# Kernel tuning notes

Measured on AMD Instinct MI355X. Metric: run time of the kernel, lower is better.

## Reference

```python
import jax, jax.numpy as jnp
import numpy as np

N = 100000   # nodes
E = 800000   # directed edges (before self-loops)
D = 256      # in_feats == out_feats


def setup_inputs() -> dict:
    key = jax.random.key(0)
    ks = jax.random.split(key, 6)
    scale = 1.0 / np.sqrt(D)
    features = jax.random.normal(ks[0], (N, D), dtype=jnp.float32)
    src = jax.random.randint(ks[1], (E,), 0, N, dtype=jnp.int32)
    dst = jax.random.randint(ks[2], (E,), 0, N, dtype=jnp.int32)
    W1 = jax.random.normal(ks[3], (D, D), dtype=jnp.float32) * scale
    b1 = jnp.zeros((D,), dtype=jnp.float32)
    W2 = jax.random.normal(ks[4], (D, D), dtype=jnp.float32) * scale
    b2 = jnp.zeros((D,), dtype=jnp.float32)
    return {"features": features, "src": src, "dst": dst,
            "W1": W1, "b1": b1, "W2": W2, "b2": b2}


def _graph_conv(h, src, dst, norm_src, norm_dst, W, b):
    # DGL GraphConv, norm='both': out = D_in^{-1/2} A (D_out^{-1/2} h W) + b
    h = (h * norm_src) @ W            # [N, D] project (W first; in==out)
    agg = jax.ops.segment_sum(h[src], dst, num_segments=N)  # SpMM gather-scatter
    return agg * norm_dst + b


def reference(features, src, dst, W1, b1, W2, b2):
    # forward does g = dgl.add_self_loop(g)
    loops = jnp.arange(N, dtype=src.dtype)
    s = jnp.concatenate([src, loops])
    d = jnp.concatenate([dst, loops])
    ones = jnp.ones_like(s, dtype=jnp.float32)
    deg_out = jax.ops.segment_sum(ones, s, num_segments=N)   # out-degree (src side)
    deg_in = jax.ops.segment_sum(ones, d, num_segments=N)    # in-degree  (dst side)
    norm_src = jnp.where(deg_out > 0, deg_out ** -0.5, 0.0)[:, None]
    norm_dst = jnp.where(deg_in > 0, deg_in ** -0.5, 0.0)[:, None]
    x = _graph_conv(features, s, d, norm_src, norm_dst, W1, b1)
    x = jax.nn.relu(x)
    x = _graph_conv(x, s, d, norm_src, norm_dst, W2, b2)
    return x
```

## Files before the change

### kernel.cpp

```cpp
#include <hip/hip_runtime.h>

#define NN 100000
#define DD 256
#define SCAN_BLK 1024

typedef unsigned int uint;
typedef unsigned short ushort;
typedef __attribute__((ext_vector_type(8))) short bfx8;
typedef __attribute__((ext_vector_type(4))) float fx4;

__device__ __forceinline__ ushort f2bf(float f) {
    uint u = __float_as_uint(f);
    u += 0x7fff + ((u >> 16) & 1);
    return (ushort)(u >> 16);
}

__device__ __forceinline__ uint cvtpk(float lo, float hi) {
    uint r;
    asm("v_cvt_pk_bf16_f32 %0, %1, %2" : "=v"(r) : "v"(lo), "v"(hi));
    return r;
}

__global__ __launch_bounds__(256) void k_count(const int* __restrict__ src,
                                               const int* __restrict__ dst, int E,
                                               int* __restrict__ dego,
                                               int* __restrict__ degi) {
    int e = blockIdx.x * 256 + threadIdx.x;
    if (e < E) {
        atomicAdd(&dego[src[e]], 1);
        atomicAdd(&degi[dst[e]], 1);
    }
}

__global__ __launch_bounds__(256) void k_norm(const int* __restrict__ dego,
                                              const int* __restrict__ degi,
                                              float* __restrict__ ns,
                                              float* __restrict__ nd) {
    int i = blockIdx.x * 256 + threadIdx.x;
    if (i < NN) {
        ns[i] = rsqrtf((float)(dego[i] + 1));
        nd[i] = rsqrtf((float)(degi[i] + 1));
    }
}

__device__ __forceinline__ int block_scan_inc(int v, int* sm) {
    int t = threadIdx.x;
    sm[t] = v;
    __syncthreads();
    for (int o = 1; o < SCAN_BLK; o <<= 1) {
        int x = (t >= o) ? sm[t - o] : 0;
        __syncthreads();
        sm[t] += x;
        __syncthreads();
    }
    return sm[t];
}

__global__ __launch_bounds__(SCAN_BLK) void k_scan1(const int* __restrict__ degi,
                                                    int* __restrict__ partials) {
    __shared__ int sm[SCAN_BLK];
    int i = blockIdx.x * SCAN_BLK + threadIdx.x;
    int v = (i < NN) ? degi[i] : 0;
    block_scan_inc(v, sm);
    if (threadIdx.x == 0) partials[blockIdx.x] = sm[SCAN_BLK - 1];
}

__global__ __launch_bounds__(128) void k_scan2(int* __restrict__ partials, int nb) {
    __shared__ int sm[128];
    int t = threadIdx.x;
    int v = (t < nb) ? partials[t] : 0;
    sm[t] = v;
    __syncthreads();
    for (int o = 1; o < 128; o <<= 1) {
        int x = (t >= o) ? sm[t - o] : 0;
        __syncthreads();
        sm[t] += x;
        __syncthreads();
    }
    if (t < nb) partials[t] = sm[t] - v;
}

__global__ __launch_bounds__(SCAN_BLK) void k_scan3(const int* __restrict__ degi,
                                                    const int* __restrict__ partials,
                                                    int* __restrict__ rowptr,
                                                    int* __restrict__ cursor) {
    __shared__ int sm[SCAN_BLK];
    int i = blockIdx.x * SCAN_BLK + threadIdx.x;
    int v = (i < NN) ? degi[i] : 0;
    int incl = block_scan_inc(v, sm);
    int excl = partials[blockIdx.x] + incl - v;
    if (i <= NN) rowptr[i] = excl;
    if (i < NN) cursor[i] = excl;
}

__global__ __launch_bounds__(256) void k_fill(const int* __restrict__ src,
                                              const int* __restrict__ dst, int E,
                                              int* __restrict__ cursor,
                                              int* __restrict__ eidx) {
    int e = blockIdx.x * 256 + threadIdx.x;
    if (e < E) {
        int d = dst[e];
        int p = atomicAdd(&cursor[d], 1);
        eidx[p] = src[e];
    }
}

__global__ __launch_bounds__(256) void k_convW(const float* __restrict__ W1,
                                               const float* __restrict__ W2,
                                               ushort* __restrict__ Wt1,
                                               ushort* __restrict__ Wt2) {
    int n = blockIdx.x & 255, k = threadIdx.x;
    const float* W = (blockIdx.x < 256) ? W1 : W2;
    ushort* Wt = (blockIdx.x < 256) ? Wt1 : Wt2;
    Wt[n * DD + k] = f2bf(W[(size_t)k * DD + n]);
}

template <bool FP32A>
__global__ __launch_bounds__(512, 4) void k_mfgemm(const void* __restrict__ Av,
                                                   const float* __restrict__ nrm,
                                                   const ushort* __restrict__ Wt,
                                                   ushort* __restrict__ H) {
    constexpr int CPR = FP32A ? 16 : 8;
    constexpr int CALLS = (128 * CPR) / (8 * 64);
    __shared__ uint4 atq[2][128 * CPR];
    int t = threadIdx.x;
    int brow = blockIdx.x * 128;
    int lane = t & 63, w = t >> 6;
    int wr = w >> 2, wc = w & 3;
    int lg = lane >> 4, lr = lane & 15;

    uint gofs[CALLS];
#pragma unroll
    for (int i = 0; i < CALLS; ++i) {
        int slot = (w * CALLS + i) * 64;
        int r = slot / CPR + lane / CPR;
        int cs = (lane % CPR) ^ (r & 7);
        int row = brow + r;
        if (row >= NN) row = NN - 1;
        if (FP32A)
            gofs[i] = (uint)(((size_t)row * DD + cs * 4) * 4);
        else
            gofs[i] = (uint)(((size_t)row * DD + cs * 8) * 2);
    }

    auto stage = [&](int buf, int ks) {
#pragma unroll
        for (int i = 0; i < CALLS; ++i) {
            int slot = (w * CALLS + i) * 64;
            const char* g = (const char*)Av + gofs[i] + ks * (FP32A ? 256 : 128);
            __builtin_amdgcn_global_load_lds(
                (const __attribute__((address_space(1))) uint*)g,
                (__attribute__((address_space(3))) uint*)&atq[buf][slot], 16, 0, 0);
        }
    };

    const uint4* wb[4];
#pragma unroll
    for (int ni = 0; ni < 4; ++ni)
        wb[ni] = (const uint4*)(Wt + (size_t)(wc * 64 + ni * 16 + lr) * DD);

    bfx8 bfr2[2][4];
    auto ldB = [&](int ks) {
#pragma unroll
        for (int kk = 0; kk < 2; ++kk)
#pragma unroll
            for (int ni = 0; ni < 4; ++ni)
                bfr2[kk][ni] = *(const bfx8*)&wb[ni][ks * 8 + kk * 4 + lg];
    };

    fx4 acc[4][4];
#pragma unroll
    for (int mi = 0; mi < 4; ++mi)
#pragma unroll
        for (int ni = 0; ni < 4; ++ni)
            acc[mi][ni] = (fx4){0.f, 0.f, 0.f, 0.f};

    stage(0, 0);
    ldB(0);
    __syncthreads();

    int buf = 0;
#pragma unroll
    for (int ks = 0; ks < 4; ++ks) {
        if (ks < 3) stage(buf ^ 1, ks + 1);
#pragma unroll
        for (int kk = 0; kk < 2; ++kk) {
#pragma unroll
            for (int mi = 0; mi < 4; ++mi) {
                int r = wr * 64 + mi * 16 + lr;
                bfx8 af;
                if (FP32A) {
                    int cf = (kk * 4 + lg) * 2;
                    fx4 q0 = *(const fx4*)&atq[buf][r * 16 + (cf ^ (r & 7))];
                    fx4 q1 = *(const fx4*)&atq[buf][r * 16 + ((cf + 1) ^ (r & 7))];
                    uint4 uu;
                    uu.x = cvtpk(q0.x, q0.y);
                    uu.y = cvtpk(q0.z, q0.w);
                    uu.z = cvtpk(q1.x, q1.y);
                    uu.w = cvtpk(q1.z, q1.w);
                    af = *(bfx8*)&uu;
                } else {
                    int c = kk * 4 + lg;
                    af = *(const bfx8*)&atq[buf][r * 8 + (c ^ (r & 7))];
                }
#pragma unroll
                for (int ni = 0; ni < 4; ++ni)
                    acc[mi][ni] = __builtin_amdgcn_mfma_f32_16x16x32_bf16(
                        af, bfr2[kk][ni], acc[mi][ni], 0, 0, 0);
            }
        }
        if (ks < 3) ldB(ks + 1);
        __syncthreads();
        buf ^= 1;
    }

    float scl[4][4];
    if (FP32A) {
#pragma unroll
        for (int mi = 0; mi < 4; ++mi)
#pragma unroll
            for (int j = 0; j < 4; ++j) {
                int row = brow + wr * 64 + mi * 16 + lg * 4 + j;
                scl[mi][j] = nrm[row < NN ? row : NN - 1];
            }
    }
    ushort* hs = (ushort*)&atq[0][0];
#pragma unroll
    for (int h = 0; h < 2; ++h) {
        if (wr == h) {
#pragma unroll
            for (int mi = 0; mi < 4; ++mi)
#pragma unroll
                for (int ni = 0; ni < 4; ++ni)
#pragma unroll
                    for (int j = 0; j < 4; ++j) {
                        int rl = mi * 16 + lg * 4 + j;
                        int c = wc * 64 + ni * 16 + lr;
                        float v = acc[mi][ni][j];
                        if (FP32A) v *= scl[mi][j];
                        hs[rl * 256 + (((c >> 3) ^ (rl & 7)) << 3) + (c & 7)] =
                            f2bf(v);
                    }
        }
        __syncthreads();
        {
            int rl = t >> 3;
            int grow = brow + h * 64 + rl;
            if (grow < NN) {
                ushort* hp = H + (size_t)grow * DD;
#pragma unroll
                for (int i = 0; i < 4; ++i) {
                    int ch = (t & 7) + i * 8;
                    uint4 v = *(const uint4*)&hs[rl * 256 + ((ch ^ (rl & 7)) << 3)];
                    *(uint4*)(hp + ch * 8) = v;
                }
            }
        }
        __syncthreads();
    }
}

__global__ __launch_bounds__(256) void k_spmm_bf(const ushort* __restrict__ T,
                                                 const int* __restrict__ rowptr,
                                                 const int* __restrict__ eidx,
                                                 const float* __restrict__ nd,
                                                 const float* __restrict__ ns,
                                                 const float* __restrict__ bias,
                                                 ushort* __restrict__ obf,
                                                 float* __restrict__ of,
                                                 int layer1) {
    int wid = threadIdx.x >> 6, lane = threadIdx.x & 63;
    int node = blockIdx.x * 4 + wid;
    if (node >= NN) return;
    int c = lane << 2;
    uint2 sv = *(const uint2*)(T + (size_t)node * DD + c);
    float p0[4], p1[4], p2[4], p3[4];
    p0[0] = __uint_as_float(sv.x << 16);
    p0[1] = __uint_as_float(sv.x & 0xffff0000u);
    p0[2] = __uint_as_float(sv.y << 16);
    p0[3] = __uint_as_float(sv.y & 0xffff0000u);
#pragma unroll
    for (int j = 0; j < 4; ++j) { p1[j] = 0.f; p2[j] = 0.f; p3[j] = 0.f; }
    int e = rowptr[node], end = rowptr[node + 1];
    for (; e + 3 < end; e += 4) {
        int s0 = eidx[e], s1 = eidx[e + 1], s2 = eidx[e + 2], s3 = eidx[e + 3];
        uint2 v0 = *(const uint2*)(T + (size_t)s0 * DD + c);
        uint2 v1 = *(const uint2*)(T + (size_t)s1 * DD + c);
        uint2 v2 = *(const uint2*)(T + (size_t)s2 * DD + c);
        uint2 v3 = *(const uint2*)(T + (size_t)s3 * DD + c);
        p0[0] += __uint_as_float(v0.x << 16);
        p0[1] += __uint_as_float(v0.x & 0xffff0000u);
        p0[2] += __uint_as_float(v0.y << 16);
        p0[3] += __uint_as_float(v0.y & 0xffff0000u);
        p1[0] += __uint_as_float(v1.x << 16);
        p1[1] += __uint_as_float(v1.x & 0xffff0000u);
        p1[2] += __uint_as_float(v1.y << 16);
        p1[3] += __uint_as_float(v1.y & 0xffff0000u);
        p2[0] += __uint_as_float(v2.x << 16);
        p2[1] += __uint_as_float(v2.x & 0xffff0000u);
        p2[2] += __uint_as_float(v2.y << 16);
        p2[3] += __uint_as_float(v2.y & 0xffff0000u);
        p3[0] += __uint_as_float(v3.x << 16);
        p3[1] += __uint_as_float(v3.x & 0xffff0000u);
        p3[2] += __uint_as_float(v3.y << 16);
        p3[3] += __uint_as_float(v3.y & 0xffff0000u);
    }
    for (; e < end; ++e) {
        int s0 = eidx[e];
        uint2 v0 = *(const uint2*)(T + (size_t)s0 * DD + c);
        p0[0] += __uint_as_float(v0.x << 16);
        p0[1] += __uint_as_float(v0.x & 0xffff0000u);
        p0[2] += __uint_as_float(v0.y << 16);
        p0[3] += __uint_as_float(v0.y & 0xffff0000u);
    }
#pragma unroll
    for (int j = 0; j < 4; ++j) p0[j] += (p1[j] + p2[j]) + p3[j];
    float n = nd[node];
    float4 bb = *(const float4*)(bias + c);
    float o0 = fmaf(p0[0], n, bb.x);
    float o1 = fmaf(p0[1], n, bb.y);
    float o2 = fmaf(p0[2], n, bb.z);
    float o3 = fmaf(p0[3], n, bb.w);
    if (layer1) {
        float s = ns[node];
        o0 = fmaxf(o0, 0.f) * s; o1 = fmaxf(o1, 0.f) * s;
        o2 = fmaxf(o2, 0.f) * s; o3 = fmaxf(o3, 0.f) * s;
        uint lo = (uint)f2bf(o0) | ((uint)f2bf(o1) << 16);
        uint hi = (uint)f2bf(o2) | ((uint)f2bf(o3) << 16);
        *(uint2*)(obf + (size_t)node * DD + c) = make_uint2(lo, hi);
    } else {
        fx4 o = {o0, o1, o2, o3};
        __builtin_nontemporal_store(o, (fx4*)(of + (size_t)node * DD + c));
    }
}

extern "C" void kernel_launch(void* const* d_in, const int* in_sizes, int n_in,
                              void* d_out, int out_size, void* d_ws, size_t ws_size,
                              hipStream_t stream) {
    const float* features = (const float*)d_in[0];
    const int* src = (const int*)d_in[1];
    const int* dst = (const int*)d_in[2];
    const float* W1 = (const float*)d_in[3];
    const float* b1 = (const float*)d_in[4];
    const float* W2 = (const float*)d_in[5];
    const float* b2 = (const float*)d_in[6];
    int E = in_sizes[1];
    float* out = (float*)d_out;

    size_t off = 0;
    auto alloc = [&](size_t nbytes) -> void* {
        void* p = (char*)d_ws + off;
        off += (nbytes + 255) & ~(size_t)255;
        return p;
    };
    int* dego = (int*)alloc((size_t)NN * 4);
    int* degi = (int*)alloc((size_t)NN * 4);
    float* norm_src = (float*)alloc((size_t)NN * 4);
    float* norm_dst = (float*)alloc((size_t)NN * 4);
    int* rowptr = (int*)alloc((size_t)(NN + 1) * 4);
    int* cursor = (int*)alloc((size_t)NN * 4);
    int* partials = (int*)alloc(128 * 4);
    int* eidx = (int*)alloc((size_t)E * 4);
    ushort* Wt1 = (ushort*)alloc((size_t)DD * DD * 2);
    ushort* Wt2 = (ushort*)alloc((size_t)DD * DD * 2);
    ushort* Xbf = (ushort*)alloc((size_t)NN * DD * 2);
    ushort* Hbf = (ushort*)alloc((size_t)NN * DD * 2);

    const int NB = (NN + SCAN_BLK - 1) / SCAN_BLK;

    hipMemsetAsync(dego, 0, (size_t)2 * 400128, stream);
    k_count<<<(E + 255) / 256, 256, 0, stream>>>(src, dst, E, dego, degi);
    k_norm<<<(NN + 255) / 256, 256, 0, stream>>>(dego, degi, norm_src, norm_dst);
    k_scan1<<<NB, SCAN_BLK, 0, stream>>>(degi, partials);
    k_scan2<<<1, 128, 0, stream>>>(partials, NB);
    k_scan3<<<NB, SCAN_BLK, 0, stream>>>(degi, partials, rowptr, cursor);
    k_fill<<<(E + 255) / 256, 256, 0, stream>>>(src, dst, E, cursor, eidx);
    k_convW<<<512, 256, 0, stream>>>(W1, W2, Wt1, Wt2);

    dim3 ggrid((NN + 127) / 128);
    k_mfgemm<true><<<ggrid, 512, 0, stream>>>(features, norm_src, Wt1, Hbf);
    k_spmm_bf<<<(NN + 3) / 4, 256, 0, stream>>>(Hbf, rowptr, eidx, norm_dst,
                                                norm_src, b1, Xbf, out, 1);
    k_mfgemm<false><<<ggrid, 512, 0, stream>>>(Xbf, nullptr, Wt2, Hbf);
    k_spmm_bf<<<(NN + 3) / 4, 256, 0, stream>>>(Hbf, rowptr, eidx, norm_dst,
                                                norm_src, b2, nullptr, out, 0);
}
```

Measured before the change: 398.3 us.

## Fuse prep kernels, pre-swizzle W into MFMA fragment order, register-stage fp32 A

Folds the degree-normalisation kernel into the first scan pass. The weight bf16 conversion is merged into the scan2 launch and now writes weights directly in MFMA B-fragment order, so each lane loads its B fragments contiguously. The fp32 GEMM path now loads A through registers, converts to bf16 once, and stores bf16 into shared memory, instead of staging fp32 via direct-to-LDS loads and converting per MFMA read. This cuts two launches and halves the LDS footprint for the first GEMM, at the cost of register-staged global loads that may overlap less well with compute.

```diff
diff --git a/kernel.cpp b/kernel.cpp
--- a/kernel.cpp
+++ b/kernel.cpp
@@ -32,17 +32,6 @@
     }
 }
 
-__global__ __launch_bounds__(256) void k_norm(const int* __restrict__ dego,
-                                              const int* __restrict__ degi,
-                                              float* __restrict__ ns,
-                                              float* __restrict__ nd) {
-    int i = blockIdx.x * 256 + threadIdx.x;
-    if (i < NN) {
-        ns[i] = rsqrtf((float)(dego[i] + 1));
-        nd[i] = rsqrtf((float)(degi[i] + 1));
-    }
-}
-
 __device__ __forceinline__ int block_scan_inc(int v, int* sm) {
     int t = threadIdx.x;
     sm[t] = v;
@@ -56,28 +45,62 @@
     return sm[t];
 }
 
-__global__ __launch_bounds__(SCAN_BLK) void k_scan1(const int* __restrict__ degi,
-                                                    int* __restrict__ partials) {
+__global__ __launch_bounds__(SCAN_BLK) void k_scan1n(const int* __restrict__ degi,
+                                                     const int* __restrict__ dego,
+                                                     int* __restrict__ partials,
+                                                     float* __restrict__ ns,
+                                                     float* __restrict__ nd) {
     __shared__ int sm[SCAN_BLK];
     int i = blockIdx.x * SCAN_BLK + threadIdx.x;
     int v = (i < NN) ? degi[i] : 0;
+    if (i < NN) {
+        ns[i] = rsqrtf((float)(dego[i] + 1));
+        nd[i] = rsqrtf((float)(v + 1));
+    }
     block_scan_inc(v, sm);
     if (threadIdx.x == 0) partials[blockIdx.x] = sm[SCAN_BLK - 1];
 }
 
-__global__ __launch_bounds__(128) void k_scan2(int* __restrict__ partials, int nb) {
-    __shared__ int sm[128];
-    int t = threadIdx.x;
-    int v = (t < nb) ? partials[t] : 0;
-    sm[t] = v;
-    __syncthreads();
-    for (int o = 1; o < 128; o <<= 1) {
-        int x = (t >= o) ? sm[t - o] : 0;
-        __syncthreads();
-        sm[t] += x;
-        __syncthreads();
-    }
-    if (t < nb) partials[t] = sm[t] - v;
+__global__ __launch_bounds__(256) void k_scan2cw(int* __restrict__ partials, int nb,
+                                                 const float* __restrict__ W1,
+                                                 const float* __restrict__ W2,
+                                                 ushort* __restrict__ Wf1,
+                                                 ushort* __restrict__ Wf2) {
+    if (blockIdx.x == 0) {
+        __shared__ int sm[128];
+        int t = threadIdx.x;
+        int v = (t < 128 && t < nb) ? partials[t] : 0;
+        if (t < 128) sm[t] = v;
+        __syncthreads();
+        for (int o = 1; o < 128; o <<= 1) {
+            int x = (t < 128 && t >= o) ? sm[t - o] : 0;
+            __syncthreads();
+            if (t < 128) sm[t] += x;
+            __syncthreads();
+        }
+        if (t < nb) partials[t] = sm[t] - v;
+    } else {
+        int tid = (blockIdx.x - 1) * 256 + threadIdx.x;
+        int m = tid >> 13;
+        int r = tid & 8191;
+        int lane = r & 63;
+        int kf = (r >> 6) & 7;
+        int c16 = r >> 9;
+        int n = c16 * 16 + (lane & 15);
+        int kb = kf * 32 + (lane >> 4) * 8;
+        const float* W = m ? W2 : W1;
+        ushort* Wf = m ? Wf2 : Wf1;
+        uint4 u;
+        u.x = (uint)f2bf(W[(size_t)(kb + 0) * DD + n]) |
+              ((uint)f2bf(W[(size_t)(kb + 1) * DD + n]) << 16);
+        u.y = (uint)f2bf(W[(size_t)(kb + 2) * DD + n]) |
+              ((uint)f2bf(W[(size_t)(kb + 3) * DD + n]) << 16);
+        u.z = (uint)f2bf(W[(size_t)(kb + 4) * DD + n]) |
+              ((uint)f2bf(W[(size_t)(kb + 5) * DD + n]) << 16);
+        u.w = (uint)f2bf(W[(size_t)(kb + 6) * DD + n]) |
+              ((uint)f2bf(W[(size_t)(kb + 7) * DD + n]) << 16);
+        *(uint4*)&Wf[(size_t)r * 8] = u;
+    }
 }
 
 __global__ __launch_bounds__(SCAN_BLK) void k_scan3(const int* __restrict__ degi,
@@ -105,67 +128,80 @@
     }
 }
 
-__global__ __launch_bounds__(256) void k_convW(const float* __restrict__ W1,
-                                               const float* __restrict__ W2,
-                                               ushort* __restrict__ Wt1,
-                                               ushort* __restrict__ Wt2) {
-    int n = blockIdx.x & 255, k = threadIdx.x;
-    const float* W = (blockIdx.x < 256) ? W1 : W2;
-    ushort* Wt = (blockIdx.x < 256) ? Wt1 : Wt2;
-    Wt[n * DD + k] = f2bf(W[(size_t)k * DD + n]);
-}
-
 template <bool FP32A>
 __global__ __launch_bounds__(512, 4) void k_mfgemm(const void* __restrict__ Av,
                                                    const float* __restrict__ nrm,
-                                                   const ushort* __restrict__ Wt,
+                                                   const ushort* __restrict__ Wf,
                                                    ushort* __restrict__ H) {
-    constexpr int CPR = FP32A ? 16 : 8;
-    constexpr int CALLS = (128 * CPR) / (8 * 64);
-    __shared__ uint4 atq[2][128 * CPR];
+    __shared__ uint4 atq[2][128 * 8];
     int t = threadIdx.x;
     int brow = blockIdx.x * 128;
     int lane = t & 63, w = t >> 6;
     int wr = w >> 2, wc = w & 3;
     int lg = lane >> 4, lr = lane & 15;
 
-    uint gofs[CALLS];
-#pragma unroll
-    for (int i = 0; i < CALLS; ++i) {
-        int slot = (w * CALLS + i) * 64;
-        int r = slot / CPR + lane / CPR;
-        int cs = (lane % CPR) ^ (r & 7);
-        int row = brow + r;
-        if (row >= NN) row = NN - 1;
-        if (FP32A)
-            gofs[i] = (uint)(((size_t)row * DD + cs * 4) * 4);
-        else
+    int sr = t >> 3, sc = t & 7;
+    int rows_[2];
+#pragma unroll
+    for (int i = 0; i < 2; ++i) {
+        int r = brow + sr + i * 64;
+        rows_[i] = (r < NN) ? r : NN - 1;
+    }
+    float4 svf[2][2];
+    uint gofs[2];
+    if (!FP32A) {
+#pragma unroll
+        for (int i = 0; i < 2; ++i) {
+            int slot = (w * 2 + i) * 64;
+            int r = slot / 8 + lane / 8;
+            int cs = (lane & 7) ^ (r & 7);
+            int row = brow + r;
+            if (row >= NN) row = NN - 1;
             gofs[i] = (uint)(((size_t)row * DD + cs * 8) * 2);
-    }
-
+        }
+    }
+
+    auto ldA = [&](int ks) {
+        const float* X = (const float*)Av;
+#pragma unroll
+        for (int i = 0; i < 2; ++i) {
+            const float4* p =
+                (const float4*)(X + (size_t)rows_[i] * DD + ks * 64 + sc * 8);
+            svf[i][0] = p[0];
+            svf[i][1] = p[1];
+        }
+    };
+    auto wrA = [&](int buf) {
+#pragma unroll
+        for (int i = 0; i < 2; ++i) {
+            int r = sr + i * 64;
+            uint4 u;
+            u.x = cvtpk(svf[i][0].x, svf[i][0].y);
+            u.y = cvtpk(svf[i][0].z, svf[i][0].w);
+            u.z = cvtpk(svf[i][1].x, svf[i][1].y);
+            u.w = cvtpk(svf[i][1].z, svf[i][1].w);
+            atq[buf][r * 8 + (sc ^ (r & 7))] = u;
+        }
+    };
     auto stage = [&](int buf, int ks) {
 #pragma unroll
-        for (int i = 0; i < CALLS; ++i) {
-            int slot = (w * CALLS + i) * 64;
-            const char* g = (const char*)Av + gofs[i] + ks * (FP32A ? 256 : 128);
+        for (int i = 0; i < 2; ++i) {
+            int slot = (w * 2 + i) * 64;
+            const char* g = (const char*)Av + gofs[i] + ks * 128;
             __builtin_amdgcn_global_load_lds(
                 (const __attribute__((address_space(1))) uint*)g,
                 (__attribute__((address_space(3))) uint*)&atq[buf][slot], 16, 0, 0);
         }
     };
 
-    const uint4* wb[4];
-#pragma unroll
-    for (int ni = 0; ni < 4; ++ni)
-        wb[ni] = (const uint4*)(Wt + (size_t)(wc * 64 + ni * 16 + lr) * DD);
-
     bfx8 bfr2[2][4];
     auto ldB = [&](int ks) {
 #pragma unroll
         for (int kk = 0; kk < 2; ++kk)
 #pragma unroll
             for (int ni = 0; ni < 4; ++ni)
-                bfr2[kk][ni] = *(const bfx8*)&wb[ni][ks * 8 + kk * 4 + lg];
+                bfr2[kk][ni] = *(const bfx8*)&Wf[
+                    (((size_t)(wc * 4 + ni) * 8 + (ks * 2 + kk)) * 64 + lane) * 8];
     };
 
     fx4 acc[4][4];
@@ -175,41 +211,34 @@
         for (int ni = 0; ni < 4; ++ni)
             acc[mi][ni] = (fx4){0.f, 0.f, 0.f, 0.f};
 
-    stage(0, 0);
+    if (FP32A) { ldA(0); wrA(0); } else stage(0, 0);
     ldB(0);
     __syncthreads();
 
     int buf = 0;
 #pragma unroll
     for (int ks = 0; ks < 4; ++ks) {
-        if (ks < 3) stage(buf ^ 1, ks + 1);
+        if (ks < 3) {
+            if (FP32A) ldA(ks + 1);
+            else stage(buf ^ 1, ks + 1);
+        }
 #pragma unroll
         for (int kk = 0; kk < 2; ++kk) {
 #pragma unroll
             for (int mi = 0; mi < 4; ++mi) {
                 int r = wr * 64 + mi * 16 + lr;
-                bfx8 af;
-                if (FP32A) {
-                    int cf = (kk * 4 + lg) * 2;
-                    fx4 q0 = *(const fx4*)&atq[buf][r * 16 + (cf ^ (r & 7))];
-                    fx4 q1 = *(const fx4*)&atq[buf][r * 16 + ((cf + 1) ^ (r & 7))];
-                    uint4 uu;
-                    uu.x = cvtpk(q0.x, q0.y);
-                    uu.y = cvtpk(q0.z, q0.w);
-                    uu.z = cvtpk(q1.x, q1.y);
-                    uu.w = cvtpk(q1.z, q1.w);
-                    af = *(bfx8*)&uu;
-                } else {
-                    int c = kk * 4 + lg;
-                    af = *(const bfx8*)&atq[buf][r * 8 + (c ^ (r & 7))];
-                }
+                int c = kk * 4 + lg;
+                bfx8 af = *(const bfx8*)&atq[buf][r * 8 + (c ^ (r & 7))];
 #pragma unroll
                 for (int ni = 0; ni < 4; ++ni)
                     acc[mi][ni] = __builtin_amdgcn_mfma_f32_16x16x32_bf16(
                         af, bfr2[kk][ni], acc[mi][ni], 0, 0, 0);
             }
         }
-        if (ks < 3) ldB(ks + 1);
+        if (ks < 3) {
+            if (FP32A) wrA(buf ^ 1);
+            ldB(ks + 1);
+        }
         __syncthreads();
         buf ^= 1;
     }
@@ -361,8 +390,8 @@
     int* cursor = (int*)alloc((size_t)NN * 4);
     int* partials = (int*)alloc(128 * 4);
     int* eidx = (int*)alloc((size_t)E * 4);
-    ushort* Wt1 = (ushort*)alloc((size_t)DD * DD * 2);
-    ushort* Wt2 = (ushort*)alloc((size_t)DD * DD * 2);
+    ushort* Wf1 = (ushort*)alloc((size_t)DD * DD * 2);
+    ushort* Wf2 = (ushort*)alloc((size_t)DD * DD * 2);
     ushort* Xbf = (ushort*)alloc((size_t)NN * DD * 2);
     ushort* Hbf = (ushort*)alloc((size_t)NN * DD * 2);
 
@@ -370,18 +399,16 @@
 
     hipMemsetAsync(dego, 0, (size_t)2 * 400128, stream);
     k_count<<<(E + 255) / 256, 256, 0, stream>>>(src, dst, E, dego, degi);
-    k_norm<<<(NN + 255) / 256, 256, 0, stream>>>(dego, degi, norm_src, norm_dst);
-    k_scan1<<<NB, SCAN_BLK, 0, stream>>>(degi, partials);
-    k_scan2<<<1, 128, 0, stream>>>(partials, NB);
+    k_scan1n<<<NB, SCAN_BLK, 0, stream>>>(degi, dego, partials, norm_src, norm_dst);
+    k_scan2cw<<<65, 256, 0, stream>>>(partials, NB, W1, W2, Wf1, Wf2);
     k_scan3<<<NB, SCAN_BLK, 0, stream>>>(degi, partials, rowptr, cursor);
     k_fill<<<(E + 255) / 256, 256, 0, stream>>>(src, dst, E, cursor, eidx);
-    k_convW<<<512, 256, 0, stream>>>(W1, W2, Wt1, Wt2);
 
     dim3 ggrid((NN + 127) / 128);
-    k_mfgemm<true><<<ggrid, 512, 0, stream>>>(features, norm_src, Wt1, Hbf);
+    k_mfgemm<true><<<ggrid, 512, 0, stream>>>(features, norm_src, Wf1, Hbf);
     k_spmm_bf<<<(NN + 3) / 4, 256, 0, stream>>>(Hbf, rowptr, eidx, norm_dst,
                                                 norm_src, b1, Xbf, out, 1);
-    k_mfgemm<false><<<ggrid, 512, 0, stream>>>(Xbf, nullptr, Wt2, Hbf);
+    k_mfgemm<false><<<ggrid, 512, 0, stream>>>(Xbf, nullptr, Wf2, Hbf);
     k_spmm_bf<<<(NN + 3) / 4, 256, 0, stream>>>(Hbf, rowptr, eidx, norm_dst,
                                                 norm_src, b2, nullptr, out, 0);
 }
```

Result: faster. 358.7 us (-9.9%).
